# Kernel tuning notes

Measured on AMD Instinct MI355X. Metric: run time of the kernel, lower is better.

Reference implementation:

```python
import jax, jax.numpy as jnp
import numpy as np

B, P, G, H, W = 4, 16384, 512, 512, 512


def setup_inputs() -> dict:
    key = jax.random.key(0)
    k1, k2, k3 = jax.random.split(key, 3)
    # point coordinates live in pixel space [0, W) x [0, H)
    pred_points = jax.random.uniform(k1, (B, P, 2), jnp.float32) * jnp.float32(W)
    gt_points = jax.random.uniform(k2, (B, G, 2), jnp.float32) * jnp.float32(W)
    # label map values: 0 = background, 1..G = instance ids
    label_maps = jax.random.randint(k3, (B, H, W), 0, G + 1, jnp.int32)
    return {"pred_points": pred_points, "gt_points": gt_points, "label_maps": label_maps}


def reference(pred_points, gt_points, label_maps):
    """Faithful vectorized PointsMasksMatcher forward.

    Instead of materializing one-hot masks [G,H,W] and doing masks[:, y, x],
    we gather the label at each rounded point location and compare with the
    instance id (identical math: one_hot(label)[j+1, y, x] > 0  <=>
    label[y, x] == j+1).

    Returns (src_idx [B,G] int32, tgt_idx [B,G] int32, costs [B,G] float32).
    tgt is simply arange(G) per batch (every gt j gets matched), matching the
    original which appends exactly one pair per gt.
    """
    Bn, Pn, _ = pred_points.shape
    Gn = gt_points.shape[1]
    Hn, Wn = label_maps.shape[1:]

    coords = jnp.round(pred_points).astype(jnp.int32)          # [B,P,2] (x,y)
    x = jnp.clip(coords[..., 0], 0, Wn - 1)
    y = jnp.clip(coords[..., 1], 0, Hn - 1)
    # label of each pred point's pixel: [B,P]
    point_labels = jax.vmap(lambda lm, yy, xx: lm[yy, xx])(label_maps, y, x)
    # inside[b,p,j] = point p lies inside mask j  (label == j+1)
    inside = point_labels[:, :, None] == jnp.arange(1, Gn + 1, dtype=point_labels.dtype)[None, None, :]  # [B,P,G]

    # pairwise euclidean distances (cdist): [B,P,G]
    diff = pred_points[:, :, None, :] - gt_points[:, None, :, :]
    D = jnp.sqrt(jnp.sum(diff * diff, axis=-1))

    has_inside = jnp.any(inside, axis=1)                       # [B,G]
    INF = jnp.asarray(jnp.inf, D.dtype)
    D_inside = jnp.where(inside, D, INF)
    # if mask j has >=1 inside point: argmin over inside points; else argmin over all
    D_sel = jnp.where(has_inside[:, None, :], D_inside, D)     # [B,P,G]

    src = jnp.argmin(D_sel, axis=1).astype(jnp.int32)          # [B,G]
    costs = jnp.min(D_sel, axis=1)                             # [B,G]
    tgt = jnp.broadcast_to(jnp.arange(Gn, dtype=jnp.int32)[None, :], (Bn, Gn))
    return src, tgt, costs
```

## Files before the change

### kernel.cpp

```cpp
#include <hip/hip_runtime.h>
#include <math.h>

#define BB 4
#define PP 16384
#define GG 512
#define HH 512
#define WW 512
#define GPB 8
#define BPB 64
#define NTHR2 512
#define CAPL 128

__device__ __forceinline__ float distf(float px, float py, float gx, float gy) {
#pragma clang fp contract(off)
    float dx = px - gx;
    float dy = py - gy;
    float a = dx * dx;
    float c = dy * dy;
    return sqrtf(a + c);
}

__global__ void k_label(const float* __restrict__ pred, const int* __restrict__ lm,
                        int* __restrict__ labels) {
    int t = blockIdx.x * blockDim.x + threadIdx.x;
    int b = t >> 14;
    float px = pred[2 * t + 0];
    float py = pred[2 * t + 1];
    int x = min(max((int)rintf(px), 0), WW - 1);
    int y = min(max((int)rintf(py), 0), HH - 1);
    labels[t] = lm[((b << 9) + y) * WW + x];
}

__global__ void __launch_bounds__(NTHR2) k_match(const float* __restrict__ pred,
                                                 const float* __restrict__ gt,
                                                 const int* __restrict__ labels,
                                                 float* __restrict__ out) {
    __shared__ int cnt[GPB];
    __shared__ int bidx[GPB][CAPL];

    const int b     = blockIdx.x / BPB;
    const int gbase = (blockIdx.x % BPB) * GPB;
    const int tid   = threadIdx.x;

    if (tid < GPB) cnt[tid] = 0;
    __syncthreads();

    const float* predb = pred + (size_t)b * PP * 2;
    const int*   labb  = labels + (size_t)b * PP;

    const int4* lab4 = (const int4*)labb;
    #pragma unroll
    for (int i = tid; i < PP / 4; i += NTHR2) {
        int4 lv = lab4[i];
        int p0 = i * 4;
        int lg;
        lg = lv.x - 1 - gbase; if ((unsigned)lg < GPB) { int s = atomicAdd(&cnt[lg], 1); if (s < CAPL) bidx[lg][s] = p0 + 0; }
        lg = lv.y - 1 - gbase; if ((unsigned)lg < GPB) { int s = atomicAdd(&cnt[lg], 1); if (s < CAPL) bidx[lg][s] = p0 + 1; }
        lg = lv.z - 1 - gbase; if ((unsigned)lg < GPB) { int s = atomicAdd(&cnt[lg], 1); if (s < CAPL) bidx[lg][s] = p0 + 2; }
        lg = lv.w - 1 - gbase; if ((unsigned)lg < GPB) { int s = atomicAdd(&cnt[lg], 1); if (s < CAPL) bidx[lg][s] = p0 + 3; }
    }
    __syncthreads();

    const int w    = tid >> 6;
    const int lane = tid & 63;
    const int g    = gbase + w;
    const float gx = gt[(size_t)(b * GG + g) * 2 + 0];
    const float gy = gt[(size_t)(b * GG + g) * 2 + 1];
    const int n = cnt[w];

    float bd = INFINITY;
    int   bi = 0x7fffffff;

    if (n == 0) {
        for (int p = lane; p < PP; p += 64) {
            float d = distf(predb[2 * p], predb[2 * p + 1], gx, gy);
            if (d < bd || (d == bd && p < bi)) { bd = d; bi = p; }
        }
    } else if (n <= CAPL) {
        for (int e = lane; e < n; e += 64) {
            int p = bidx[w][e];
            float d = distf(predb[2 * p], predb[2 * p + 1], gx, gy);
            if (d < bd || (d == bd && p < bi)) { bd = d; bi = p; }
        }
    } else {
        for (int p = lane; p < PP; p += 64) {
            if (labb[p] == g + 1) {
                float d = distf(predb[2 * p], predb[2 * p + 1], gx, gy);
                if (d < bd || (d == bd && p < bi)) { bd = d; bi = p; }
            }
        }
    }

    for (int off = 32; off > 0; off >>= 1) {
        float od = __shfl_xor(bd, off, 64);
        int   oi = __shfl_xor(bi, off, 64);
        if (od < bd || (od == bd && oi < bi)) { bd = od; bi = oi; }
    }

    if (lane == 0) {
        int o = b * GG + g;
        out[o]               = (float)bi;
        out[BB * GG + o]     = (float)g;
        out[2 * BB * GG + o] = bd;
    }
}

extern "C" void kernel_launch(void* const* d_in, const int* in_sizes, int n_in,
                              void* d_out, int out_size, void* d_ws, size_t ws_size,
                              hipStream_t stream) {
    const float* pred = (const float*)d_in[0];
    const float* gt   = (const float*)d_in[1];
    const int*   lm   = (const int*)d_in[2];
    float* out = (float*)d_out;
    int* labels = (int*)d_ws;

    k_label<<<dim3(BB * PP / 256), dim3(256), 0, stream>>>(pred, lm, labels);
    k_match<<<dim3(BB * BPB), dim3(NTHR2), 0, stream>>>(pred, gt, labels, out);
}
```

Baseline: 15.74 us.

## Store labels as u16 and double gts per block to cut label rescans

Labels are narrowed from int32 to 16-bit, which halves the intermediate buffer and the bytes each block streams when building per-gt candidate lists. Each match block now handles 16 gts with 1024 threads, so every block scans the label array once for twice as many gts and the total label traffic drops. Point coordinates are loaded as float2. The trade-off is half as many blocks (128 instead of 256), which may underfill the GPU, and more contention on the shared-memory atomics per block.

```diff
diff --git a/kernel.cpp b/kernel.cpp
--- a/kernel.cpp
+++ b/kernel.cpp
@@ -6,10 +6,13 @@
 #define GG 512
 #define HH 512
 #define WW 512
-#define GPB 8
-#define BPB 64
-#define NTHR2 512
+#define GPB 16
+#define BPB 32
+#define NTHR2 1024
 #define CAPL 128
+
+typedef unsigned short u16;
+typedef __attribute__((ext_vector_type(8))) unsigned short u16x8;
 
 __device__ __forceinline__ float distf(float px, float py, float gx, float gy) {
 #pragma clang fp contract(off)
@@ -21,19 +24,19 @@
 }
 
 __global__ void k_label(const float* __restrict__ pred, const int* __restrict__ lm,
-                        int* __restrict__ labels) {
+                        u16* __restrict__ labels) {
     int t = blockIdx.x * blockDim.x + threadIdx.x;
     int b = t >> 14;
     float px = pred[2 * t + 0];
     float py = pred[2 * t + 1];
     int x = min(max((int)rintf(px), 0), WW - 1);
     int y = min(max((int)rintf(py), 0), HH - 1);
-    labels[t] = lm[((b << 9) + y) * WW + x];
+    labels[t] = (u16)lm[((b << 9) + y) * WW + x];
 }
 
 __global__ void __launch_bounds__(NTHR2) k_match(const float* __restrict__ pred,
                                                  const float* __restrict__ gt,
-                                                 const int* __restrict__ labels,
+                                                 const u16* __restrict__ labels,
                                                  float* __restrict__ out) {
     __shared__ int cnt[GPB];
     __shared__ int bidx[GPB][CAPL];
@@ -45,19 +48,22 @@
     if (tid < GPB) cnt[tid] = 0;
     __syncthreads();
 
-    const float* predb = pred + (size_t)b * PP * 2;
-    const int*   labb  = labels + (size_t)b * PP;
+    const float2* predb = (const float2*)(pred + (size_t)b * PP * 2);
+    const u16*    labb  = labels + (size_t)b * PP;
 
-    const int4* lab4 = (const int4*)labb;
+    const u16x8* lab8 = (const u16x8*)labb;
     #pragma unroll
-    for (int i = tid; i < PP / 4; i += NTHR2) {
-        int4 lv = lab4[i];
-        int p0 = i * 4;
-        int lg;
-        lg = lv.x - 1 - gbase; if ((unsigned)lg < GPB) { int s = atomicAdd(&cnt[lg], 1); if (s < CAPL) bidx[lg][s] = p0 + 0; }
-        lg = lv.y - 1 - gbase; if ((unsigned)lg < GPB) { int s = atomicAdd(&cnt[lg], 1); if (s < CAPL) bidx[lg][s] = p0 + 1; }
-        lg = lv.z - 1 - gbase; if ((unsigned)lg < GPB) { int s = atomicAdd(&cnt[lg], 1); if (s < CAPL) bidx[lg][s] = p0 + 2; }
-        lg = lv.w - 1 - gbase; if ((unsigned)lg < GPB) { int s = atomicAdd(&cnt[lg], 1); if (s < CAPL) bidx[lg][s] = p0 + 3; }
+    for (int i = tid; i < PP / 8; i += NTHR2) {
+        u16x8 lv = lab8[i];
+        int p0 = i * 8;
+        #pragma unroll
+        for (int j = 0; j < 8; ++j) {
+            int lg = (int)lv[j] - 1 - gbase;
+            if ((unsigned)lg < GPB) {
+                int s = atomicAdd(&cnt[lg], 1);
+                if (s < CAPL) bidx[lg][s] = p0 + j;
+            }
+        }
     }
     __syncthreads();
 
@@ -73,19 +79,22 @@
 
     if (n == 0) {
         for (int p = lane; p < PP; p += 64) {
-            float d = distf(predb[2 * p], predb[2 * p + 1], gx, gy);
+            float2 c = predb[p];
+            float d = distf(c.x, c.y, gx, gy);
             if (d < bd || (d == bd && p < bi)) { bd = d; bi = p; }
         }
     } else if (n <= CAPL) {
         for (int e = lane; e < n; e += 64) {
             int p = bidx[w][e];
-            float d = distf(predb[2 * p], predb[2 * p + 1], gx, gy);
+            float2 c = predb[p];
+            float d = distf(c.x, c.y, gx, gy);
             if (d < bd || (d == bd && p < bi)) { bd = d; bi = p; }
         }
     } else {
         for (int p = lane; p < PP; p += 64) {
-            if (labb[p] == g + 1) {
-                float d = distf(predb[2 * p], predb[2 * p + 1], gx, gy);
+            if ((int)labb[p] == g + 1) {
+                float2 c = predb[p];
+                float d = distf(c.x, c.y, gx, gy);
                 if (d < bd || (d == bd && p < bi)) { bd = d; bi = p; }
             }
         }
@@ -112,7 +121,7 @@
     const float* gt   = (const float*)d_in[1];
     const int*   lm   = (const int*)d_in[2];
     float* out = (float*)d_out;
-    int* labels = (int*)d_ws;
+    u16* labels = (u16*)d_ws;
 
     k_label<<<dim3(BB * PP / 256), dim3(256), 0, stream>>>(pred, lm, labels);
     k_match<<<dim3(BB * BPB), dim3(NTHR2), 0, stream>>>(pred, gt, labels, out);
```

Measured after the change: 14.46 us. -8.1%, faster.
